# Performance work log

Hardware: AMD Instinct MI355X
Metric: run time of the kernel (lower is better)

Reference implementation:

```python
import jax, jax.numpy as jnp
import numpy as np
import math

NUM_HEADS = 16
NUM_BUCKETS = 32
MAX_DISTANCE = 128


def _relative_position_bucket(relative_position, num_buckets=NUM_BUCKETS, max_distance=MAX_DISTANCE):
    num_buckets = num_buckets // 2
    ret = (relative_position >= 0).astype(jnp.int32) * num_buckets
    n = jnp.abs(relative_position)
    max_exact = num_buckets // 2
    is_small = n < max_exact
    # guard log(0); masked by is_small anyway
    n_safe = jnp.maximum(n, 1).astype(jnp.float32)
    val_if_large = max_exact + (
        jnp.log(n_safe / max_exact) / math.log(max_distance / max_exact) * (num_buckets - max_exact)
    ).astype(jnp.int32)
    val_if_large = jnp.minimum(val_if_large, num_buckets - 1)
    return ret + jnp.where(is_small, n, val_if_large)


def compute_bias(rel_bias, query_length, key_length):
    ctx = jnp.arange(query_length)[:, None]
    mem = jnp.arange(key_length)[None, :]
    rp = mem - ctx  # [Q, K]
    bucket = _relative_position_bucket(rp)  # [Q, K]
    values = rel_bias[bucket]  # [Q, K, H]
    return jnp.transpose(values, (2, 0, 1))[None]  # [1, H, Q, K]


def setup_inputs() -> dict:
    key = jax.random.key(0)
    ks = jax.random.split(key, 6)
    B, S, D = 2, 2048, 1024
    sd = 1.0 / math.sqrt(D)
    return {
        "x": jax.random.normal(ks[0], (B, S, D), jnp.float32),
        "wq": jax.random.normal(ks[1], (D, D), jnp.float32) * sd,
        "wk": jax.random.normal(ks[2], (D, D), jnp.float32) * sd,
        "wv": jax.random.normal(ks[3], (D, D), jnp.float32) * sd,
        "wo": jax.random.normal(ks[4], (D, D), jnp.float32) * sd,
        "rel_bias": jax.random.normal(ks[5], (NUM_BUCKETS, NUM_HEADS), jnp.float32),
    }


def reference(x, wq, wk, wv, wo, rel_bias):
    B, S, _ = x.shape
    inner_dim = wq.shape[0]
    head_dim = inner_dim // NUM_HEADS
    # nn.Linear stores weight as [out, in]: y = x @ W^T
    q = (x @ wq.T).reshape(B, S, NUM_HEADS, head_dim).transpose(0, 2, 1, 3)
    k = (x @ wk.T).reshape(B, S, NUM_HEADS, head_dim).transpose(0, 2, 1, 3)
    v = (x @ wv.T).reshape(B, S, NUM_HEADS, head_dim).transpose(0, 2, 1, 3)
    scores = jnp.einsum('bhqd,bhkd->bhqk', q, k) / math.sqrt(head_dim)
    past_bias = compute_bias(rel_bias, S, S)  # [1, H, S, S]
    scores = scores + past_bias
    attn_weights = jax.nn.softmax(scores, axis=-1)
    attn_output = jnp.einsum('bhqk,bhkd->bhqd', attn_weights, v)
    attn_output = attn_output.transpose(0, 2, 1, 3).reshape(B, S, inner_dim)
    attn_output = attn_output @ wo.T
    return (attn_output, past_bias)
```

## Files before the change

### kernel.cpp

```cpp
#include <hip/hip_runtime.h>

typedef __bf16 bf16_t;
typedef __bf16 bf16x8 __attribute__((ext_vector_type(8)));
typedef float  f32x4  __attribute__((ext_vector_type(4)));
typedef float  f32x4u __attribute__((ext_vector_type(4), aligned(4)));

#define ASYNC16(g, l) __builtin_amdgcn_global_load_lds( \
    (const __attribute__((address_space(1))) void*)(g), \
    (__attribute__((address_space(3))) void*)(l), 16, 0, 0)

#define MFMA(a, b, c) __builtin_amdgcn_mfma_f32_16x16x32_bf16(a, b, c, 0, 0, 0)

__global__ __launch_bounds__(256) void cast_all(
    const float* __restrict__ x, const float* __restrict__ wq,
    const float* __restrict__ wk, const float* __restrict__ wv,
    const float* __restrict__ wo,
    bf16_t* __restrict__ xb, bf16_t* __restrict__ wqkvb, bf16_t* __restrict__ wob)
{
  int i4 = blockIdx.x * 256 + threadIdx.x;
  int base = i4 * 4;
  const float* src; bf16_t* dst;
  if (base < 4194304) { src = x + base; dst = xb + base; }
  else {
    int j = base - 4194304;
    int w = j >> 20, o = j & 1048575;
    if      (w == 0) { src = wq + o; dst = wqkvb + o; }
    else if (w == 1) { src = wk + o; dst = wqkvb + (1 << 20) + o; }
    else if (w == 2) { src = wv + o; dst = wqkvb + (2 << 20) + o; }
    else             { src = wo + o; dst = wob + o; }
  }
  float4 v = *(const float4*)src;
  union { bf16_t h[4]; uint2 u; } pk;
  pk.h[0] = (bf16_t)v.x; pk.h[1] = (bf16_t)v.y;
  pk.h[2] = (bf16_t)v.z; pk.h[3] = (bf16_t)v.w;
  *(uint2*)dst = pk.u;
}

__global__ void build_tbl(const float* __restrict__ rel_bias,
                          float* __restrict__ tblB, float* __restrict__ tblE)
{
  int i = blockIdx.x * 256 + threadIdx.x;
  if (i >= 4095 * 16) return;
  int rpi = i >> 4;
  int h = i & 15;
  int rp = rpi - 2047;
  int ret = rp >= 0 ? 16 : 0;
  int n = rp < 0 ? -rp : rp;
  int b;
  if (n < 8) b = ret + n;
  else {
    double v = 2.0 * (log2((double)n) - 3.0);
    int bi = 8 + (int)v;
    b = ret + (bi < 15 ? bi : 15);
  }
  float v = rel_bias[b * 16 + h];
  tblB[h * 4096 + rpi] = v;
  tblE[h * 4096 + rpi] = v * 1.4426950408889634f;
}

__global__ __launch_bounds__(256) void gemm_qkv(
    const bf16_t* __restrict__ A, const bf16_t* __restrict__ B,
    bf16_t* __restrict__ qk, bf16_t* __restrict__ vt)
{
  const int K = 1024;
  __shared__ bf16_t As[128 * 32];
  __shared__ bf16_t Bs[128 * 32];
  const int t = threadIdx.x;
  const int w = t >> 6, l = t & 63, ln = l & 15, quad = l >> 4;
  const int wm = (w & 1) * 64, wn = (w >> 1) * 64;
  const int m0 = blockIdx.x * 128, n0 = blockIdx.y * 128;

  f32x4 acc[4][4] = {};
  const int rA = t >> 2, c8 = (t & 3) * 8;
  const bf16_t* Ag = A + (size_t)(m0 + rA) * K + c8;
  const bf16_t* Bg = B + (size_t)(n0 + rA) * K + c8;
  const size_t K64 = (size_t)64 * K;
  bf16_t* As0 = &As[t * 8];  bf16_t* As1 = &As[2048 + t * 8];
  bf16_t* Bs0 = &Bs[t * 8];  bf16_t* Bs1 = &Bs[2048 + t * 8];

  for (int kt = 0; kt < K; kt += 32) {
    ASYNC16(Ag + kt,       As0);
    ASYNC16(Ag + kt + K64, As1);
    ASYNC16(Bg + kt,       Bs0);
    ASYNC16(Bg + kt + K64, Bs1);
    __syncthreads();
    bf16x8 a[4], b[4];
#pragma unroll
    for (int mi = 0; mi < 4; ++mi)
      a[mi] = *(const bf16x8*)&As[(wm + mi * 16 + ln) * 32 + quad * 8];
#pragma unroll
    for (int ni = 0; ni < 4; ++ni)
      b[ni] = *(const bf16x8*)&Bs[(wn + ni * 16 + ln) * 32 + quad * 8];
#pragma unroll
    for (int mi = 0; mi < 4; ++mi)
#pragma unroll
      for (int ni = 0; ni < 4; ++ni)
        acc[mi][ni] = MFMA(a[mi], b[ni], acc[mi][ni]);
    __syncthreads();
  }

  if (n0 >= 2048) {
#pragma unroll
    for (int mi = 0; mi < 4; ++mi)
#pragma unroll
      for (int ni = 0; ni < 4; ++ni) {
        int col = n0 + wn + ni * 16 + ln - 2048;
        int hh = col >> 6, dd = col & 63;
        int row = m0 + wm + mi * 16 + quad * 4;
        int bb = row >> 11, ss = row & 2047;
        union { bf16_t h4[4]; uint2 u; } pk;
#pragma unroll
        for (int j = 0; j < 4; ++j) pk.h4[j] = (bf16_t)acc[mi][ni][j];
        *(uint2*)&vt[((size_t)(bb * 16 + hh) * 64 + dd) * 2048 + ss] = pk.u;
      }
  } else {
#pragma unroll
    for (int mi = 0; mi < 4; ++mi)
#pragma unroll
      for (int ni = 0; ni < 4; ++ni) {
        int row = m0 + wm + mi * 16 + quad * 4;
        int col = n0 + wn + ni * 16 + ln;
#pragma unroll
        for (int j = 0; j < 4; ++j)
          qk[(size_t)(row + j) * 2048 + col] = (bf16_t)acc[mi][ni][j];
      }
  }
}

__global__ __launch_bounds__(256) void gemm_wo(
    const bf16_t* __restrict__ A, const bf16_t* __restrict__ B,
    float* __restrict__ C)
{
  const int K = 1024, N = 1024;
  __shared__ bf16_t As[64 * 32];
  __shared__ bf16_t Bs[128 * 32];
  const int t = threadIdx.x;
  const int w = t >> 6, l = t & 63, ln = l & 15, quad = l >> 4;
  const int wm = (w & 1) * 32, wn = (w >> 1) * 64;
  const int m0 = blockIdx.x * 64, n0 = blockIdx.y * 128;

  f32x4 acc[2][4] = {};
  const int rr = t >> 2, c8 = (t & 3) * 8;
  const bf16_t* Ag = A + (size_t)(m0 + rr) * K + c8;
  const bf16_t* Bg = B + (size_t)(n0 + rr) * K + c8;
  const size_t K64 = (size_t)64 * K;
  bf16_t* As0 = &As[t * 8];
  bf16_t* Bs0 = &Bs[t * 8];  bf16_t* Bs1 = &Bs[2048 + t * 8];

  for (int kt = 0; kt < K; kt += 32) {
    ASYNC16(Ag + kt,       As0);
    ASYNC16(Bg + kt,       Bs0);
    ASYNC16(Bg + kt + K64, Bs1);
    __syncthreads();
    bf16x8 a[2], b[4];
#pragma unroll
    for (int mi = 0; mi < 2; ++mi)
      a[mi] = *(const bf16x8*)&As[(wm + mi * 16 + ln) * 32 + quad * 8];
#pragma unroll
    for (int ni = 0; ni < 4; ++ni)
      b[ni] = *(const bf16x8*)&Bs[(wn + ni * 16 + ln) * 32 + quad * 8];
#pragma unroll
    for (int mi = 0; mi < 2; ++mi)
#pragma unroll
      for (int ni = 0; ni < 4; ++ni)
        acc[mi][ni] = MFMA(a[mi], b[ni], acc[mi][ni]);
    __syncthreads();
  }

#pragma unroll
  for (int mi = 0; mi < 2; ++mi)
#pragma unroll
    for (int ni = 0; ni < 4; ++ni) {
      int row = m0 + wm + mi * 16 + quad * 4;
      int col = n0 + wn + ni * 16 + ln;
#pragma unroll
      for (int j = 0; j < 4; ++j)
        C[(size_t)(row + j) * N + col] = acc[mi][ni][j];
    }
}

__global__ __launch_bounds__(256, 2) void flash_attn(
    const bf16_t* __restrict__ qk, const bf16_t* __restrict__ vt,
    const float* __restrict__ tblE, bf16_t* __restrict__ attn)
{
  __shared__ __align__(16) bf16_t Kt[128 * 64];
  __shared__ __align__(16) bf16_t Vs[64 * 128];
  __shared__ __align__(16) bf16_t Ps[4 * 32 * 128];
  const int t = threadIdx.x, w = t >> 6, l = t & 63, ln = l & 15, quad = l >> 4;
  const int q0 = blockIdx.x * 128, h = blockIdx.y, b = blockIdx.z;
  const int S = 2048;
  const int qa = q0 + w * 32 + ln;
  const int qb = qa + 16;

  const bf16_t* Qpa = qk + (size_t)(b * S + qa) * 2048 + h * 64 + quad * 8;
  const bf16_t* Qpb = qk + (size_t)(b * S + qb) * 2048 + h * 64 + quad * 8;
  bf16x8 bq0a = *(const bf16x8*)Qpa;
  bf16x8 bq1a = *(const bf16x8*)(Qpa + 32);
  bf16x8 bq0b = *(const bf16x8*)Qpb;
  bf16x8 bq1b = *(const bf16x8*)(Qpb + 32);

  f32x4 oa[4] = {}, ob[4] = {};
  float lia = 0.f, lib = 0.f;

  const int krow = l >> 3;
  const int kg8  = ((l & 7) ^ krow) * 8;
  const int vrow = l >> 4;
  const int vg8  = ((l & 15) ^ (w * 4 + vrow)) * 8;
  const bf16_t* Kg = qk + (size_t)(b * S) * 2048 + 1024 + h * 64 + kg8;
  const bf16_t* Vg = vt + (size_t)(b * 16 + h) * 64 * 2048 + vg8;
  const float* tba = tblE + h * 4096 + 2047 - qa;
  const float* tbb = tblE + h * 4096 + 2047 - qb;

  for (int kt = 0; kt < S; kt += 128) {
    __syncthreads();
#pragma unroll
    for (int cc = 0; cc < 4; ++cc) {
      int kr0 = w * 8 + cc * 32;
      ASYNC16(Kg + (size_t)(kt + kr0 + krow) * 2048, &Kt[kr0 * 64 + l * 8]);
      int vr0 = w * 4 + cc * 16;
      ASYNC16(Vg + (size_t)(vr0 + vrow) * 2048 + kt, &Vs[vr0 * 128 + l * 8]);
    }
    __syncthreads();

    const float* tbka = tba + kt;
    const float* tbkb = tbb + kt;
    bf16_t* pwa = &Ps[w * 4096 + ln * 128];
    bf16_t* pwb = pwa + 16 * 128;
#pragma unroll
    for (int f = 0; f < 8; ++f) {
      const bf16_t* kp = &Kt[(f * 16 + ln) * 64];
      bf16x8 a0 = *(const bf16x8*)(kp + ((quad ^ (ln & 7)) * 8));
      bf16x8 a1 = *(const bf16x8*)(kp + (((4 + quad) ^ (ln & 7)) * 8));
      f32x4 acca = {}, accb = {};
      acca = MFMA(a0, bq0a, acca);
      acca = MFMA(a1, bq1a, acca);
      accb = MFMA(a0, bq0b, accb);
      accb = MFMA(a1, bq1b, accb);
      f32x4u bva = *(const f32x4u*)(tbka + f * 16 + quad * 4);
      f32x4u bvb = *(const f32x4u*)(tbkb + f * 16 + quad * 4);
      union { bf16_t h4[4]; uint2 u; } pka, pkb;
#pragma unroll
      for (int j = 0; j < 4; ++j) {
        float pa = __builtin_amdgcn_exp2f(fmaf(acca[j], 0.18033688011112042f, bva[j]));
        float pb = __builtin_amdgcn_exp2f(fmaf(accb[j], 0.18033688011112042f, bvb[j]));
        lia += pa; lib += pb;
        pka.h4[j] = (bf16_t)pa; pkb.h4[j] = (bf16_t)pb;
      }
      int po = (((2 * f + (quad >> 1)) ^ ln) * 8) + (quad & 1) * 4;
      *(uint2*)&pwa[po] = pka.u;
      *(uint2*)&pwb[po] = pkb.u;
    }

#pragma unroll
    for (int kk = 0; kk < 4; ++kk) {
      int so = ((kk * 4 + quad) ^ ln) * 8;
      bf16x8 bpa = *(const bf16x8*)&pwa[so];
      bf16x8 bpb = *(const bf16x8*)&pwb[so];
#pragma unroll
      for (int dt = 0; dt < 4; ++dt) {
        bf16x8 av = *(const bf16x8*)&Vs[(dt * 16 + ln) * 128 + so];
        oa[dt] = MFMA(av, bpa, oa[dt]);
        ob[dt] = MFMA(av, bpb, ob[dt]);
      }
    }
  }

  lia += __shfl_xor(lia, 16);
  lia += __shfl_xor(lia, 32);
  lib += __shfl_xor(lib, 16);
  lib += __shfl_xor(lib, 32);
  float inva = 1.f / lia, invb = 1.f / lib;
  bf16_t* opa = attn + (size_t)(b * S + qa) * 1024 + h * 64 + quad * 4;
  bf16_t* opb = attn + (size_t)(b * S + qb) * 1024 + h * 64 + quad * 4;
#pragma unroll
  for (int dt = 0; dt < 4; ++dt) {
    union { bf16_t h4[4]; uint2 u; } pka, pkb;
#pragma unroll
    for (int j = 0; j < 4; ++j) {
      pka.h4[j] = (bf16_t)(oa[dt][j] * inva);
      pkb.h4[j] = (bf16_t)(ob[dt][j] * invb);
    }
    *(uint2*)&opa[dt * 16] = pka.u;
    *(uint2*)&opb[dt * 16] = pkb.u;
  }
}

__global__ __launch_bounds__(256) void bias_out(const float* __restrict__ tbl,
                                                float* __restrict__ out1)
{
  int i = blockIdx.x * 256 + threadIdx.x;
  int hq = i >> 9;
  int k4 = (i & 511) * 4;
  int h = hq >> 11, q = hq & 2047;
  const float* tp = tbl + (h << 12) + (k4 - q + 2047);
  float4 v;
  v.x = __ldg(tp);     v.y = __ldg(tp + 1);
  v.z = __ldg(tp + 2); v.w = __ldg(tp + 3);
  ((float4*)out1)[i] = v;
}

extern "C" void kernel_launch(void* const* d_in, const int* in_sizes, int n_in,
                              void* d_out, int out_size, void* d_ws, size_t ws_size,
                              hipStream_t stream)
{
  const float* x  = (const float*)d_in[0];
  const float* wq = (const float*)d_in[1];
  const float* wk = (const float*)d_in[2];
  const float* wv = (const float*)d_in[3];
  const float* wo = (const float*)d_in[4];
  const float* rb = (const float*)d_in[5];
  float* out0 = (float*)d_out;
  float* out1 = out0 + 4194304;

  char* ws = (char*)d_ws;
  bf16_t* xb    = (bf16_t*)(ws);
  bf16_t* wqkvb = (bf16_t*)(ws + 8388608);
  bf16_t* wob   = (bf16_t*)(ws + 14680064);
  bf16_t* qk    = (bf16_t*)(ws + 16777216);
  bf16_t* vt    = (bf16_t*)(ws + 33554432);
  float*  tblB  = (float*)(ws + 41943040);
  float*  tblE  = (float*)(ws + 42205184);
  bf16_t* attnb = xb;

  cast_all<<<8192, 256, 0, stream>>>(x, wq, wk, wv, wo, xb, wqkvb, wob);
  build_tbl<<<256, 256, 0, stream>>>(rb, tblB, tblE);
  gemm_qkv<<<dim3(32, 24), 256, 0, stream>>>(xb, wqkvb, qk, vt);
  flash_attn<<<dim3(16, 16, 2), 256, 0, stream>>>(qk, vt, tblE, attnb);
  gemm_wo<<<dim3(64, 8), 256, 0, stream>>>(attnb, wob, out0);
  bias_out<<<65536, 256, 0, stream>>>(tblB, out1);
}
```

Baseline: 408.9 us.

## Feed softmax probabilities from registers into PV MFMA, dropping the LDS staging buffer

Removes the per-wave shared-memory buffer that held the bf16 probability tile. Each 16-key fragment of P now goes straight from registers into a 16x16x16 bf16 MFMA against the matching V slice. This removes LDS writes and reads for P and frees 32KB of LDS, so the launch bound is raised to 4 blocks per SM. The cost is twice as many half-depth MFMAs and possible register pressure under the tighter occupancy bound.

After: 521.3 us. 27.5% more time.

```diff
diff --git a/kernel.cpp b/kernel.cpp
--- a/kernel.cpp
+++ b/kernel.cpp
@@ -4,12 +4,25 @@
 typedef __bf16 bf16x8 __attribute__((ext_vector_type(8)));
 typedef float  f32x4  __attribute__((ext_vector_type(4)));
 typedef float  f32x4u __attribute__((ext_vector_type(4), aligned(4)));
+typedef short  s16x4  __attribute__((ext_vector_type(4)));
 
 #define ASYNC16(g, l) __builtin_amdgcn_global_load_lds( \
     (const __attribute__((address_space(1))) void*)(g), \
     (__attribute__((address_space(3))) void*)(l), 16, 0, 0)
 
 #define MFMA(a, b, c) __builtin_amdgcn_mfma_f32_16x16x32_bf16(a, b, c, 0, 0, 0)
+
+#if __has_builtin(__builtin_amdgcn_mfma_f32_16x16x16bf16_1k)
+#define MFMA16(a, b, c) __builtin_amdgcn_mfma_f32_16x16x16bf16_1k(a, b, c, 0, 0, 0)
+#else
+static __device__ __forceinline__ f32x4 mfma16_asm(s16x4 a, s16x4 b, f32x4 c) {
+  f32x4 d;
+  asm volatile("v_mfma_f32_16x16x16_bf16 %0, %1, %2, %3"
+               : "=v"(d) : "v"(a), "v"(b), "v"(c));
+  return d;
+}
+#define MFMA16(a, b, c) mfma16_asm(a, b, c)
+#endif
 
 __global__ __launch_bounds__(256) void cast_all(
     const float* __restrict__ x, const float* __restrict__ wq,
@@ -179,13 +192,12 @@
     }
 }
 
-__global__ __launch_bounds__(256, 2) void flash_attn(
+__global__ __launch_bounds__(256, 4) void flash_attn(
     const bf16_t* __restrict__ qk, const bf16_t* __restrict__ vt,
     const float* __restrict__ tblE, bf16_t* __restrict__ attn)
 {
   __shared__ __align__(16) bf16_t Kt[128 * 64];
   __shared__ __align__(16) bf16_t Vs[64 * 128];
-  __shared__ __align__(16) bf16_t Ps[4 * 32 * 128];
   const int t = threadIdx.x, w = t >> 6, l = t & 63, ln = l & 15, quad = l >> 4;
   const int q0 = blockIdx.x * 128, h = blockIdx.y, b = blockIdx.z;
   const int S = 2048;
@@ -224,8 +236,6 @@
 
     const float* tbka = tba + kt;
     const float* tbkb = tbb + kt;
-    bf16_t* pwa = &Ps[w * 4096 + ln * 128];
-    bf16_t* pwb = pwa + 16 * 128;
 #pragma unroll
     for (int f = 0; f < 8; ++f) {
       const bf16_t* kp = &Kt[(f * 16 + ln) * 64];
@@ -238,7 +248,7 @@
       accb = MFMA(a1, bq1b, accb);
       f32x4u bva = *(const f32x4u*)(tbka + f * 16 + quad * 4);
       f32x4u bvb = *(const f32x4u*)(tbkb + f * 16 + quad * 4);
-      union { bf16_t h4[4]; uint2 u; } pka, pkb;
+      union { bf16_t h4[4]; s16x4 s; } pka, pkb;
 #pragma unroll
       for (int j = 0; j < 4; ++j) {
         float pa = __builtin_amdgcn_exp2f(fmaf(acca[j], 0.18033688011112042f, bva[j]));
@@ -246,21 +256,12 @@
         lia += pa; lib += pb;
         pka.h4[j] = (bf16_t)pa; pkb.h4[j] = (bf16_t)pb;
       }
-      int po = (((2 * f + (quad >> 1)) ^ ln) * 8) + (quad & 1) * 4;
-      *(uint2*)&pwa[po] = pka.u;
-      *(uint2*)&pwb[po] = pkb.u;
-    }
-
-#pragma unroll
-    for (int kk = 0; kk < 4; ++kk) {
-      int so = ((kk * 4 + quad) ^ ln) * 8;
-      bf16x8 bpa = *(const bf16x8*)&pwa[so];
-      bf16x8 bpb = *(const bf16x8*)&pwb[so];
+      const int vcol = (((2 * f + (quad >> 1)) ^ ln) * 8) + (quad & 1) * 4;
 #pragma unroll
       for (int dt = 0; dt < 4; ++dt) {
-        bf16x8 av = *(const bf16x8*)&Vs[(dt * 16 + ln) * 128 + so];
-        oa[dt] = MFMA(av, bpa, oa[dt]);
-        ob[dt] = MFMA(av, bpb, ob[dt]);
+        s16x4 av = *(const s16x4*)&Vs[(dt * 16 + ln) * 128 + vcol];
+        oa[dt] = MFMA16(av, pka.s, oa[dt]);
+        ob[dt] = MFMA16(av, pkb.s, ob[dt]);
       }
     }
   }
```
